# Performance work log

Hardware: AMD Instinct MI355X
Metric: run time of the kernel (lower is better)

The kernel has to match this reference:

```python
import jax, jax.numpy as jnp
import numpy as np
from jax import lax

BN_EPS = 1e-5


def _conv(x, w, pad=0):
    # NCHW / OIHW conv, stride 1
    return lax.conv_general_dilated(
        x, w, (1, 1), [(pad, pad), (pad, pad)],
        dimension_numbers=("NCHW", "OIHW", "NCHW"))


def _bn(x, p):
    # p: [4, C] rows = gamma, beta, running_mean, running_var (eval-mode BN)
    g, b, m, v = p
    inv = g * lax.rsqrt(v + BN_EPS)
    return x * inv[None, :, None, None] + (b - m * inv)[None, :, None, None]


def _avgpool3(x):
    # AvgPool2d(k=3, stride=1, pad=1, count_include_pad=True) -> sum window / 9
    s = lax.reduce_window(x, 0.0, lax.add, (1, 1, 3, 3), (1, 1, 1, 1),
                          [(0, 0), (0, 0), (1, 1), (1, 1)])
    return s / 9.0


def setup_inputs() -> dict:
    key = jax.random.key(0)
    B, C, H, W = 8, 64, 256, 256
    mid = C // 2
    ks = jax.random.split(key, 12)

    def bn_params(k, ch):
        k1, k2, k3, k4 = jax.random.split(k, 4)
        gamma = 1.0 + 0.1 * jax.random.normal(k1, (ch,), jnp.float32)
        beta = 0.1 * jax.random.normal(k2, (ch,), jnp.float32)
        mean = 0.1 * jax.random.normal(k3, (ch,), jnp.float32)
        var = jax.random.uniform(k4, (ch,), jnp.float32, 0.5, 1.5)
        return jnp.stack([gamma, beta, mean, var])

    def w(k, shape):
        fan_in = shape[1] * shape[2] * shape[3]
        return jax.random.normal(k, shape, jnp.float32) / np.sqrt(fan_in)

    return {
        "x": jax.random.normal(ks[0], (B, C, H, W), jnp.float32),
        "w_main": w(ks[1], (mid, C, 3, 3)),
        "bn_main": bn_params(ks[2], mid),
        "w_1x1": w(ks[3], (mid, C, 1, 1)),
        "bn_1x1": bn_params(ks[4], mid),
        "w_3x3_1": w(ks[5], (mid, C, 1, 1)),
        "bn_3x3_1": bn_params(ks[6], mid),
        "w_3x3_2": w(ks[7], (mid, mid, 3, 3)),
        "bn_3x3_2": bn_params(ks[8], mid),
        "w_avg": w(ks[9], (mid, C, 1, 1)),
        "bn_avg_1": bn_params(ks[10], mid),
        "bn_avg_2": bn_params(ks[10], mid),
        "c_score": jax.random.normal(ks[11], (2 * C,), jnp.float32),
    }


def reference(x, w_main, bn_main, w_1x1, bn_1x1, w_3x3_1, bn_3x3_1,
              w_3x3_2, bn_3x3_2, w_avg, bn_avg_1, bn_avg_2, c_score):
    c = x.shape[1]
    # four branches, each -> mid = c//2 channels
    branch_main = _bn(_conv(x, w_main, pad=1), bn_main)
    branch_1x1 = _bn(_conv(x, w_1x1), bn_1x1)
    branch_3x3 = _bn(_conv(_bn(_conv(x, w_3x3_1), bn_3x3_1), w_3x3_2, pad=1), bn_3x3_2)
    branch_avg = _bn(_avgpool3(_bn(_conv(x, w_avg), bn_avg_1)), bn_avg_2)
    out = jnp.concatenate([branch_main, branch_1x1, branch_3x3, branch_avg], axis=1)  # [B, 2c, H, W]

    # top-k channel selection: output channel i = sigmoid(c_score[ind[i]]) * out[:, ind[i]]
    # (the original builds a sparse [c, 2c, 1, 1] conv weight; gather+scale is the same math)
    _, ind = lax.top_k(c_score, c)
    scale = jax.nn.sigmoid(c_score)[ind]                       # [c]
    return jnp.take(out, ind, axis=1) * scale[None, :, None, None]
```

## Files before the change

### kernel.cpp

```cpp
#include <hip/hip_runtime.h>
#include <hip/hip_bf16.h>


typedef __attribute__((ext_vector_type(8))) short bf16x8;
typedef __attribute__((ext_vector_type(16))) float f32x16;
typedef __attribute__((ext_vector_type(4))) unsigned int u32x4;

#define MFMA32(a,b,c) __builtin_amdgcn_mfma_f32_32x32x16_bf16(a,b,c,0,0,0)

#define XT_OFF   131072ull
#define T1_OFF   69877760ull
#define WS_NEED  104751104ull
#define ROWP     264
#define BROW     258

__device__ __forceinline__ unsigned short f2bf(float f) {
    union { __hip_bfloat16 h; unsigned short u; } cv;
    cv.h = __float2bfloat16(f);
    return cv.u;
}

__device__ __forceinline__ f32x16 zero16() {
    f32x16 z;
    #pragma unroll
    for (int i = 0; i < 16; i++) z[i] = 0.f;
    return z;
}

__device__ __forceinline__ int xs_addr(int pos, int byteoff) {
    return pos * 128 + (byteoff ^ (((pos >> 2) & 7) << 4));
}
__device__ __forceinline__ int t1_addr(int pos, int byteoff) {
    return pos * 64 + (byteoff ^ ((pos & 3) << 4));
}

__global__ void prep_kernel(
    const float* __restrict__ c_score,
    const float* __restrict__ w_main, const float* __restrict__ bn_main,
    const float* __restrict__ w_1x1,  const float* __restrict__ bn_1x1,
    const float* __restrict__ w_3x3_1,const float* __restrict__ bn_3x3_1,
    const float* __restrict__ w_3x3_2,const float* __restrict__ bn_3x3_2,
    const float* __restrict__ w_avg,  const float* __restrict__ bn_avg_1,
    const float* __restrict__ bn_avg_2,
    int* __restrict__ och, float* __restrict__ biasb,
    __hip_bfloat16* __restrict__ wb, unsigned char* __restrict__ ws)
{
    const int t = threadIdx.x;
    const int bid = blockIdx.x;

    if (bid >= 4) {
        int gid = (bid - 4) * 256 + t;
        unsigned short* xt = (unsigned short*)(ws + XT_OFF);
        unsigned short* t1 = (unsigned short*)(ws + T1_OFF);
        int which, c, pxid;
        if (gid < 66560) { which = 0; c = gid & 7; pxid = gid >> 3; }
        else if (gid < 99840) { int j = gid - 66560; which = 1; c = j & 3; pxid = j >> 2; }
        else return;
        int b = pxid / 1040, r = pxid - b * 1040;
        int ry, cx;
        if (r < 264)      { ry = 0;             cx = r; }
        else if (r < 528) { ry = 257;           cx = r - 264; }
        else if (r < 784) { ry = 1 + (r - 528); cx = 0; }
        else              { ry = 1 + (r - 784); cx = 257; }
        u32x4 z = {0, 0, 0, 0};
        if (which == 0) {
            size_t ch = ((size_t)(b * BROW + ry) * 8 + c) * ROWP + cx;
            *(u32x4*)(xt + ch * 8) = z;
        } else {
            size_t px = (size_t)(b * BROW + ry) * ROWP + cx;
            *(u32x4*)(t1 + px * 32 + c * 8) = z;
        }
        return;
    }

    __shared__ float ssc[128];
    __shared__ float iv[6][32];

    if (t < 128) ssc[t] = 1.f / (1.f + expf(-c_score[t]));
    if (t < 32) {
        iv[0][t] = bn_main[t]  * rsqrtf(bn_main[96+t]  + 1e-5f);
        iv[1][t] = bn_1x1[t]   * rsqrtf(bn_1x1[96+t]   + 1e-5f);
        iv[2][t] = bn_3x3_1[t] * rsqrtf(bn_3x3_1[96+t] + 1e-5f);
        iv[3][t] = bn_3x3_2[t] * rsqrtf(bn_3x3_2[96+t] + 1e-5f);
        iv[4][t] = bn_avg_1[t] * rsqrtf(bn_avg_1[96+t] + 1e-5f);
        iv[5][t] = bn_avg_2[t] * rsqrtf(bn_avg_2[96+t] + 1e-5f);
    }
    __syncthreads();

    if (bid == 0) {
        if (t < 128) {
            float sj = c_score[t];
            int r = 0;
            for (int i = 0; i < 128; i++) {
                float si = c_score[i];
                r += (si > sj) || (si == sj && i < t);
            }
            och[t] = (r < 64) ? r : -1;
        }
        if (t < 32) {
            biasb[t]     = bn_3x3_1[32+t] - bn_3x3_1[64+t]*iv[2][t];
            biasb[32+t]  = (bn_main[32+t]  - bn_main[64+t]*iv[0][t])  * ssc[t];
            biasb[64+t]  = (bn_1x1[32+t]   - bn_1x1[64+t]*iv[1][t])   * ssc[32+t];
            biasb[96+t]  = (bn_3x3_2[32+t] - bn_3x3_2[64+t]*iv[3][t]) * ssc[64+t];
            biasb[128+t] = (bn_avg_2[32+t] - bn_avg_2[64+t]*iv[5][t]) * ssc[96+t];
            float b1p = bn_avg_1[32+t] - bn_avg_1[64+t]*iv[4][t];
            biasb[160+t] = ssc[96+t] * iv[5][t] * b1p * (1.f/9.f);
        }
    } else if (bid == 1) {
        for (int i = t; i < 2048; i += 256) {
            int j = i & 7, o = (i >> 3) & 31, g = (i >> 8) & 1, s = i >> 9;
            int c = s * 16 + g * 8 + j;
            wb[i]         = __float2bfloat16(w_3x3_1[o*64+c] * iv[2][o]);
            wb[20480 + i] = __float2bfloat16(w_avg[o*64+c] * iv[4][o] * iv[5][o] * (1.f/9.f) * ssc[96+o]);
            wb[22528 + i] = __float2bfloat16(w_1x1[o*64+c] * iv[1][o] * ssc[32+o]);
        }
    } else if (bid == 2) {
        for (int i = t; i < 18432; i += 256) {
            int j = i & 7, o = (i >> 3) & 31, g = (i >> 8) & 1;
            int s = (i >> 9) & 3, tap = i >> 11;
            int c = s * 16 + g * 8 + j;
            wb[2048 + i] = __float2bfloat16(w_main[o*576 + c*9 + tap] * iv[0][o] * ssc[o]);
        }
    } else {
        for (int i = t; i < 9216; i += 256) {
            int j = i & 7, o = (i >> 3) & 31, g = (i >> 8) & 1;
            int s = (i >> 9) & 1, tap = i >> 10;
            int c = s * 16 + g * 8 + j;
            wb[24576 + i] = __float2bfloat16(w_3x3_2[o*288 + c*9 + tap] * iv[3][o] * ssc[64+o]);
        }
    }
}

__global__ __launch_bounds__(256, 8) void t_kernel(
    const float* __restrict__ x, unsigned short* __restrict__ xt)
{
    const int t = threadIdx.x;
    const int co = t >> 5, pq = t & 31;
    const int y = blockIdx.y, b = blockIdx.z;
    const int pxa = blockIdx.x * 128 + pq * 4;

    const float* xp = x + ((size_t)(b * 64 + co * 8) * 65536) + y * 256 + pxa;
    float4 f[8];
    #pragma unroll
    for (int k = 0; k < 8; k++)
        f[k] = *(const float4*)(xp + (size_t)k * 65536);

    size_t xrow = ((size_t)(b * BROW + y + 1) * 8 + co) * ROWP;
    #pragma unroll
    for (int u = 0; u < 4; u++) {
        u32x4 w;
        #pragma unroll
        for (int j = 0; j < 4; j++) {
            const float* a  = (const float*)&f[2*j];
            const float* c2 = (const float*)&f[2*j+1];
            w[j] = (unsigned)f2bf(a[u]) | ((unsigned)f2bf(c2[u]) << 16);
        }
        *(u32x4*)(xt + (xrow + pxa + u + 1) * 8) = w;
    }
}

__global__ __launch_bounds__(256, 8) void m1_kernel(
    const unsigned short* __restrict__ xt,
    const __hip_bfloat16* __restrict__ Wg,
    const float* __restrict__ biasb,
    unsigned short* __restrict__ t1g)
{
    const int t = threadIdx.x;
    const int lane = t & 63, wv = t >> 6;
    const int i31 = lane & 31, g = lane >> 5;
    const int y = blockIdx.y, b = blockIdx.z;
    const int px0 = blockIdx.x * 128, m0 = wv * 32;

    size_t rowb = (size_t)(b * BROW + y + 1) * 8;
    f32x16 acc = zero16();
    #pragma unroll
    for (int s = 0; s < 4; s++) {
        int ch = s * 2 + g;
        bf16x8 a  = *(const bf16x8*)(xt + ((rowb + ch) * ROWP + px0 + m0 + i31 + 1) * 8);
        bf16x8 bA = *(const bf16x8*)(Wg + (ch * 32 + i31) * 8);
        acc = MFMA32(a, bA, acc);
    }
    float bias = biasb[i31];
    size_t trow = (size_t)(b * BROW + y + 1) * ROWP;
    #pragma unroll
    for (int r = 0; r < 16; r++) {
        int px = m0 + (r & 3) + 8 * (r >> 2) + 4 * g;
        t1g[(trow + px0 + px + 1) * 32 + i31] = f2bf(acc[r] + bias);
    }
}

__device__ __forceinline__ void store4(float* outb, const f32x16& acc,
    const int* __restrict__ och_g, const float* __restrict__ bias32,
    int cbase, int y, int x0, int i31, int g)
{
    int rank = och_g[cbase + i31];
    if (rank < 0) return;
    float bias = bias32[i31];
    float* po = outb + (size_t)rank * 65536 + y*256 + x0 + 4*g;
    #pragma unroll
    for (int q = 0; q < 4; q++) {
        float4 v;
        v.x = acc[4*q+0] + bias;
        v.y = acc[4*q+1] + bias;
        v.z = acc[4*q+2] + bias;
        v.w = acc[4*q+3] + bias;
        *(float4*)(po + 8*q) = v;
    }
}

__device__ __forceinline__ void store4avg(float* outb, const f32x16& acc,
    const int* __restrict__ och_g, const float* __restrict__ biasb,
    int y, int x0, int i31, int g)
{
    int rank = och_g[96 + i31];
    if (rank < 0) return;
    float t2b = biasb[128 + i31];
    float b19 = biasb[160 + i31];
    float cy = 3.f - (float)(y == 0) - (float)(y == 255);
    float* po = outb + (size_t)rank * 65536 + y*256 + x0 + 4*g;
    #pragma unroll
    for (int q = 0; q < 4; q++) {
        float4 v;
        #pragma unroll
        for (int u = 0; u < 4; u++) {
            int gx = x0 + 4*g + 8*q + u;
            float cx = 3.f - (float)(gx == 0) - (float)(gx == 255);
            ((float*)&v)[u] = acc[4*q+u] + t2b + b19 * (cy * cx);
        }
        *(float4*)(po + 8*q) = v;
    }
}

__global__ __launch_bounds__(256, 2) void m2ab_kernel(
    const unsigned short* __restrict__ xt,
    const unsigned short* __restrict__ t1g,
    const __hip_bfloat16* __restrict__ Wg,
    const int* __restrict__ och_g,
    const float* __restrict__ biasb,
    float* __restrict__ out)
{
    __shared__ __align__(16) unsigned char smem[43520];

    const int t = threadIdx.x;
    const int lane = t & 63, wv = t >> 6;
    const int i31 = lane & 31, g = lane >> 5;
    const int x0 = blockIdx.x * 32, y0 = blockIdx.y * 8;
    const int zz = blockIdx.z;

    const int y_0 = y0 + 2 * wv, y_1 = y_0 + 1;
    const int r0 = 2 * wv + 1, r1 = r0 + 1;

    if (zz < 8) {
        const int b = zz;
        unsigned short* xs = (unsigned short*)smem;
        {
            u32x4 tmp[11];
            int   jj[11];
            #pragma unroll
            for (int i = 0; i < 11; i++) {
                int j = t + i * 256;
                if (j > 2719) j = 2719;
                jj[i] = j;
                int c = j / 340, rem = j - c * 340, r = rem / 34, p = rem - r * 34;
                size_t src = ((size_t)(b * BROW + y0 + r) * 8 + c) * ROWP + x0 + p;
                tmp[i] = *(const u32x4*)(xt + src * 8);
            }
            #pragma unroll
            for (int i = 0; i < 11; i++)
                *(u32x4*)(xs + (size_t)jj[i] * 8) = tmp[i];
        }
        __syncthreads();

        float* outb = out + (size_t)b * (64 * 65536);
        f32x16 aM0 = zero16(), aM1 = zero16();
        f32x16 aG0 = zero16(), aG1 = zero16();
        f32x16 aX0 = zero16(), aX1 = zero16();
        {
            bf16x8 bg[4], bx[4];
            #pragma unroll
            for (int s = 0; s < 4; s++) {
                bg[s] = *(const bf16x8*)(Wg + 20480 + ((s*2+g)*32 + i31) * 8);
                bx[s] = *(const bf16x8*)(Wg + 22528 + ((s*2+g)*32 + i31) * 8);
            }
            #pragma unroll
            for (int tap = 0; tap < 9; tap++) {
                int dy = tap / 3 - 1, dx = tap - (tap / 3) * 3 - 1;
                int pbase = i31 + dx + 1;
                #pragma unroll
                for (int s = 0; s < 4; s++) {
                    bf16x8 bm = *(const bf16x8*)(Wg + 2048 + (((tap*4+s)*2+g)*32 + i31) * 8);
                    bf16x8 a0 = *(const bf16x8*)(xs + (size_t)(((s*2+g) * 10 + r0 + dy) * 34 + pbase) * 8);
                    bf16x8 a1 = *(const bf16x8*)(xs + (size_t)(((s*2+g) * 10 + r1 + dy) * 34 + pbase) * 8);
                    aM0 = MFMA32(a0, bm, aM0);
                    aM1 = MFMA32(a1, bm, aM1);
                    aG0 = MFMA32(a0, bg[s], aG0);
                    aG1 = MFMA32(a1, bg[s], aG1);
                    if (tap == 4) {
                        aX0 = MFMA32(a0, bx[s], aX0);
                        aX1 = MFMA32(a1, bx[s], aX1);
                    }
                }
            }
        }
        store4(outb, aM0, och_g, biasb + 32, 0,  y_0, x0, i31, g);
        store4(outb, aM1, och_g, biasb + 32, 0,  y_1, x0, i31, g);
        store4(outb, aX0, och_g, biasb + 64, 32, y_0, x0, i31, g);
        store4(outb, aX1, och_g, biasb + 64, 32, y_1, x0, i31, g);
        store4avg(outb, aG0, och_g, biasb, y_0, x0, i31, g);
        store4avg(outb, aG1, och_g, biasb, y_1, x0, i31, g);
    } else {
        const int b = zz - 8;
        unsigned short* t1s = (unsigned short*)smem;
        #pragma unroll
        for (int i = 0; i < 6; i++) {
            int j = t + i * 256;
            if (j > 1359) j = 1359;
            int c4 = j & 3, pr = j >> 2;
            int r = pr / 34, p = pr - r * 34;
            size_t src = ((size_t)(b * BROW + y0 + r) * ROWP + x0 + p) * 32 + c4 * 8;
            int ci = c4 * 350 + r * 35 + p;
            *(u32x4*)(t1s + (size_t)ci * 8) = *(const u32x4*)(t1g + src);
        }
        __syncthreads();

        float* outb = out + (size_t)b * (64 * 65536);
        f32x16 aC0 = zero16(), aC1 = zero16();
        #pragma unroll
        for (int tap = 0; tap < 9; tap++) {
            int dy = tap / 3 - 1, dx = tap - (tap / 3) * 3 - 1;
            int pbase = i31 + dx + 1;
            #pragma unroll
            for (int s = 0; s < 2; s++) {
                bf16x8 bc = *(const bf16x8*)(Wg + 24576 + (((tap*2+s)*2+g)*32 + i31) * 8);
                bf16x8 a0 = *(const bf16x8*)(t1s + (size_t)((s*2+g) * 350 + (r0 + dy) * 35 + pbase) * 8);
                bf16x8 a1 = *(const bf16x8*)(t1s + (size_t)((s*2+g) * 350 + (r1 + dy) * 35 + pbase) * 8);
                aC0 = MFMA32(a0, bc, aC0);
                aC1 = MFMA32(a1, bc, aC1);
            }
        }
        store4(outb, aC0, och_g, biasb + 96, 64, y_0, x0, i31, g);
        store4(outb, aC1, och_g, biasb + 96, 64, y_1, x0, i31, g);
    }
}

__global__ __launch_bounds__(512, 4) void fused_fallback(
    const float* __restrict__ x,
    const __hip_bfloat16* __restrict__ Wg,
    const int* __restrict__ och_g,
    const float* __restrict__ biasb,
    float* __restrict__ out)
{
    __shared__ __align__(16) unsigned char xs[400 * 128];
    __shared__ __align__(16) unsigned char t1s[340 * 64];

    const int t = threadIdx.x;
    const int lane = t & 63, wv = t >> 6;
    const int i31 = lane & 31, g = lane >> 5;
    const int x0 = blockIdx.x * 32, y0 = blockIdx.y * 8;
    const int b = blockIdx.z;

    const float* xb = x + (size_t)b * (64 * 65536);
    for (int j = t; j < 800; j += 512) {
        int co = j / 100;
        int rem = j - co * 100;
        int row = rem / 10, xq = rem - row * 10;
        int gy = y0 - 1 + row;
        int gx0 = x0 - 4 + 4 * xq;
        bool ok = ((unsigned)gy < 256u) && ((unsigned)gx0 <= 252u);
        const float* p = xb + (size_t)(co * 8) * 65536 + (size_t)gy * 256 + gx0;
        float4 f0 = {0,0,0,0}, f1 = {0,0,0,0}, f2 = {0,0,0,0}, f3 = {0,0,0,0};
        float4 f4 = {0,0,0,0}, f5 = {0,0,0,0}, f6 = {0,0,0,0}, f7 = {0,0,0,0};
        if (ok) {
            f0 = *(const float4*)(p);
            f1 = *(const float4*)(p + 65536);
            f2 = *(const float4*)(p + 131072);
            f3 = *(const float4*)(p + 196608);
            f4 = *(const float4*)(p + 262144);
            f5 = *(const float4*)(p + 327680);
            f6 = *(const float4*)(p + 393216);
            f7 = *(const float4*)(p + 458752);
        }
        const float* fv[8] = {(const float*)&f0, (const float*)&f1, (const float*)&f2,
                              (const float*)&f3, (const float*)&f4, (const float*)&f5,
                              (const float*)&f6, (const float*)&f7};
        #pragma unroll
        for (int u = 0; u < 4; u++) {
            int pos = row * 40 + 4 * xq + u;
            u32x4 w;
            w[0] = (unsigned)f2bf(fv[0][u]) | ((unsigned)f2bf(fv[1][u]) << 16);
            w[1] = (unsigned)f2bf(fv[2][u]) | ((unsigned)f2bf(fv[3][u]) << 16);
            w[2] = (unsigned)f2bf(fv[4][u]) | ((unsigned)f2bf(fv[5][u]) << 16);
            w[3] = (unsigned)f2bf(fv[6][u]) | ((unsigned)f2bf(fv[7][u]) << 16);
            *(u32x4*)(xs + xs_addr(pos, co * 16)) = w;
        }
    }
    __syncthreads();

    {
        bf16x8 bA[4];
        #pragma unroll
        for (int s = 0; s < 4; s++)
            bA[s] = *(const bf16x8*)(Wg + ((s*2+g)*32 + i31) * 8);
        float biasA = biasb[i31];
        for (int mt = wv; mt < 11; mt += 8) {
            int m0 = mt * 32;
            f32x16 acc = zero16();
            int qr = m0 + i31; if (qr > 339) qr = 339;
            int hy = qr / 34, hx = qr - hy * 34;
            int pos = hy * 40 + hx + 3;
            #pragma unroll
            for (int s = 0; s < 4; s++) {
                bf16x8 a = *(const bf16x8*)(xs + xs_addr(pos, s * 32 + g * 16));
                acc = MFMA32(a, bA[s], acc);
            }
            #pragma unroll
            for (int r = 0; r < 16; r++) {
                int q = m0 + (r & 3) + 8 * (r >> 2) + 4 * g;
                if (q < 340) {
                    int hy2 = q / 34, hx2 = q - hy2 * 34;
                    int gy = y0 - 1 + hy2, gx = x0 - 1 + hx2;
                    bool valid = ((unsigned)gy < 256u) && ((unsigned)gx < 256u);
                    float vv = valid ? (acc[r] + biasA) : 0.f;
                    *(unsigned short*)(t1s + t1_addr(q, i31 * 2)) = f2bf(vv);
                }
            }
        }
    }
    __syncthreads();

    float* outb = out + (size_t)b * (64 * 65536);
    const int y = y0 + wv;

    f32x16 aM = zero16(), aG = zero16(), aX = zero16();
    {
        bf16x8 bg[4], bx[4];
        #pragma unroll
        for (int s = 0; s < 4; s++) {
            bg[s] = *(const bf16x8*)(Wg + 20480 + ((s*2+g)*32 + i31) * 8);
            bx[s] = *(const bf16x8*)(Wg + 22528 + ((s*2+g)*32 + i31) * 8);
        }
        for (int tap = 0; tap < 9; tap++) {
            int dy = tap / 3 - 1, dx = tap - (tap / 3) * 3 - 1;
            int pos = (wv + 1 + dy) * 40 + 4 + dx + i31;
            #pragma unroll
            for (int s = 0; s < 4; s++) {
                bf16x8 bm = *(const bf16x8*)(Wg + 2048 + (((tap*4+s)*2+g)*32 + i31) * 8);
                bf16x8 a = *(const bf16x8*)(xs + xs_addr(pos, s * 32 + g * 16));
                aM = MFMA32(a, bm, aM);
                aG = MFMA32(a, bg[s], aG);
                if (tap == 4) aX = MFMA32(a, bx[s], aX);
            }
        }
    }
    store4(outb, aM, och_g, biasb + 32, 0,  y, x0, i31, g);
    store4(outb, aX, och_g, biasb + 64, 32, y, x0, i31, g);
    store4avg(outb, aG, och_g, biasb, y, x0, i31, g);

    f32x16 aC = zero16();
    for (int tap = 0; tap < 9; tap++) {
        int dy = tap / 3 - 1, dx = tap - (tap / 3) * 3 - 1;
        int q = (wv + 1 + dy) * 34 + 1 + dx + i31;
        #pragma unroll
        for (int s = 0; s < 2; s++) {
            bf16x8 bc = *(const bf16x8*)(Wg + 24576 + (((tap*2+s)*2+g)*32 + i31) * 8);
            bf16x8 a = *(const bf16x8*)(t1s + t1_addr(q, s * 32 + g * 16));
            aC = MFMA32(a, bc, aC);
        }
    }
    store4(outb, aC, och_g, biasb + 96, 64, y, x0, i31, g);
}

extern "C" void kernel_launch(void* const* d_in, const int* in_sizes, int n_in,
                              void* d_out, int out_size, void* d_ws, size_t ws_size,
                              hipStream_t stream)
{
    const float* x        = (const float*)d_in[0];
    const float* w_main   = (const float*)d_in[1];
    const float* bn_main  = (const float*)d_in[2];
    const float* w_1x1    = (const float*)d_in[3];
    const float* bn_1x1   = (const float*)d_in[4];
    const float* w_3x3_1  = (const float*)d_in[5];
    const float* bn_3x3_1 = (const float*)d_in[6];
    const float* w_3x3_2  = (const float*)d_in[7];
    const float* bn_3x3_2 = (const float*)d_in[8];
    const float* w_avg    = (const float*)d_in[9];
    const float* bn_avg_1 = (const float*)d_in[10];
    const float* bn_avg_2 = (const float*)d_in[11];
    const float* c_score  = (const float*)d_in[12];

    int*   och   = (int*)d_ws;
    float* biasb = (float*)((char*)d_ws + 512);
    __hip_bfloat16* wb = (__hip_bfloat16*)((char*)d_ws + 2048);

    const bool big = (ws_size >= WS_NEED);
    prep_kernel<<<big ? 394 : 4, 256, 0, stream>>>(
        c_score, w_main, bn_main, w_1x1, bn_1x1,
        w_3x3_1, bn_3x3_1, w_3x3_2, bn_3x3_2, w_avg, bn_avg_1, bn_avg_2,
        och, biasb, wb, (unsigned char*)d_ws);

    if (big) {
        unsigned short* xt  = (unsigned short*)((char*)d_ws + XT_OFF);
        unsigned short* t1g = (unsigned short*)((char*)d_ws + T1_OFF);

        t_kernel<<<dim3(2, 256, 8), 256, 0, stream>>>(x, xt);
        m1_kernel<<<dim3(2, 256, 8), 256, 0, stream>>>(xt, wb, biasb, t1g);
        m2ab_kernel<<<dim3(8, 32, 16), 256, 0, stream>>>(
            xt, t1g, wb, och, biasb, (float*)d_out);
    } else {
        fused_fallback<<<dim3(8, 32, 8), 512, 0, stream>>>(
            x, wb, och, biasb, (float*)d_out);
    }
}
```

Before: 143.6 us.

## Move halo zeroing into producer kernels, interleave m2ab branches, raise occupancy

Halo-border zeroing of the transposed input and t1 buffers moves out of the prep kernel and into t_kernel and m1_kernel, so prep launches only 4 blocks. m2ab now interleaves the two branch types by batch (even z for main/1x1/avg, odd z for the 3x3 branch), which mixes heavy and light blocks during scheduling. Its launch bounds rise from 2 to 3 blocks per CU, which may force register spills in the heavy branch.

After: 142.7 us. About the same (-0.6%).

```diff
diff --git a/kernel.cpp b/kernel.cpp
--- a/kernel.cpp
+++ b/kernel.cpp
@@ -43,35 +43,10 @@
     const float* __restrict__ w_avg,  const float* __restrict__ bn_avg_1,
     const float* __restrict__ bn_avg_2,
     int* __restrict__ och, float* __restrict__ biasb,
-    __hip_bfloat16* __restrict__ wb, unsigned char* __restrict__ ws)
+    __hip_bfloat16* __restrict__ wb)
 {
     const int t = threadIdx.x;
     const int bid = blockIdx.x;
-
-    if (bid >= 4) {
-        int gid = (bid - 4) * 256 + t;
-        unsigned short* xt = (unsigned short*)(ws + XT_OFF);
-        unsigned short* t1 = (unsigned short*)(ws + T1_OFF);
-        int which, c, pxid;
-        if (gid < 66560) { which = 0; c = gid & 7; pxid = gid >> 3; }
-        else if (gid < 99840) { int j = gid - 66560; which = 1; c = j & 3; pxid = j >> 2; }
-        else return;
-        int b = pxid / 1040, r = pxid - b * 1040;
-        int ry, cx;
-        if (r < 264)      { ry = 0;             cx = r; }
-        else if (r < 528) { ry = 257;           cx = r - 264; }
-        else if (r < 784) { ry = 1 + (r - 528); cx = 0; }
-        else              { ry = 1 + (r - 784); cx = 257; }
-        u32x4 z = {0, 0, 0, 0};
-        if (which == 0) {
-            size_t ch = ((size_t)(b * BROW + ry) * 8 + c) * ROWP + cx;
-            *(u32x4*)(xt + ch * 8) = z;
-        } else {
-            size_t px = (size_t)(b * BROW + ry) * ROWP + cx;
-            *(u32x4*)(t1 + px * 32 + c * 8) = z;
-        }
-        return;
-    }
 
     __shared__ float ssc[128];
     __shared__ float iv[6][32];
@@ -157,6 +132,23 @@
         }
         *(u32x4*)(xt + (xrow + pxa + u + 1) * 8) = w;
     }
+
+    if (blockIdx.x == 0) {
+        u32x4 z = {0, 0, 0, 0};
+        if (t < 16) {
+            int c = t & 7, side = t >> 3;
+            size_t ch = ((size_t)(b * BROW + y + 1) * 8 + c) * ROWP + (side ? 257 : 0);
+            *(u32x4*)(xt + ch * 8) = z;
+        }
+        if (y < 2) {
+            int ry = (y == 0) ? 0 : 257;
+            for (int j = t; j < 2112; j += 256) {
+                int c = j / 264, cx = j - c * 264;
+                size_t ch = ((size_t)(b * BROW + ry) * 8 + c) * ROWP + cx;
+                *(u32x4*)(xt + ch * 8) = z;
+            }
+        }
+    }
 }
 
 __global__ __launch_bounds__(256, 8) void m1_kernel(
@@ -186,6 +178,23 @@
     for (int r = 0; r < 16; r++) {
         int px = m0 + (r & 3) + 8 * (r >> 2) + 4 * g;
         t1g[(trow + px0 + px + 1) * 32 + i31] = f2bf(acc[r] + bias);
+    }
+
+    if (blockIdx.x == 0) {
+        u32x4 z = {0, 0, 0, 0};
+        if (t < 8) {
+            int c4 = t & 3, side = t >> 2;
+            size_t px = (size_t)(b * BROW + y + 1) * ROWP + (side ? 257 : 0);
+            *(u32x4*)(t1g + px * 32 + c4 * 8) = z;
+        }
+        if (y < 2) {
+            int ry = (y == 0) ? 0 : 257;
+            for (int j = t; j < 1056; j += 256) {
+                int pxi = j >> 2, c4 = j & 3;
+                size_t px = (size_t)(b * BROW + ry) * ROWP + pxi;
+                *(u32x4*)(t1g + px * 32 + c4 * 8) = z;
+            }
+        }
     }
 }
 
@@ -231,7 +240,7 @@
     }
 }
 
-__global__ __launch_bounds__(256, 2) void m2ab_kernel(
+__global__ __launch_bounds__(256, 3) void m2ab_kernel(
     const unsigned short* __restrict__ xt,
     const unsigned short* __restrict__ t1g,
     const __hip_bfloat16* __restrict__ Wg,
@@ -246,12 +255,12 @@
     const int i31 = lane & 31, g = lane >> 5;
     const int x0 = blockIdx.x * 32, y0 = blockIdx.y * 8;
     const int zz = blockIdx.z;
+    const int b = zz >> 1;
 
     const int y_0 = y0 + 2 * wv, y_1 = y_0 + 1;
     const int r0 = 2 * wv + 1, r1 = r0 + 1;
 
-    if (zz < 8) {
-        const int b = zz;
+    if ((zz & 1) == 0) {
         unsigned short* xs = (unsigned short*)smem;
         {
             u32x4 tmp[11];
@@ -309,7 +318,6 @@
         store4avg(outb, aG0, och_g, biasb, y_0, x0, i31, g);
         store4avg(outb, aG1, och_g, biasb, y_1, x0, i31, g);
     } else {
-        const int b = zz - 8;
         unsigned short* t1s = (unsigned short*)smem;
         #pragma unroll
         for (int i = 0; i < 6; i++) {
@@ -492,13 +500,12 @@
     float* biasb = (float*)((char*)d_ws + 512);
     __hip_bfloat16* wb = (__hip_bfloat16*)((char*)d_ws + 2048);
 
-    const bool big = (ws_size >= WS_NEED);
-    prep_kernel<<<big ? 394 : 4, 256, 0, stream>>>(
+    prep_kernel<<<4, 256, 0, stream>>>(
         c_score, w_main, bn_main, w_1x1, bn_1x1,
         w_3x3_1, bn_3x3_1, w_3x3_2, bn_3x3_2, w_avg, bn_avg_1, bn_avg_2,
-        och, biasb, wb, (unsigned char*)d_ws);
-
-    if (big) {
+        och, biasb, wb);
+
+    if (ws_size >= WS_NEED) {
         unsigned short* xt  = (unsigned short*)((char*)d_ws + XT_OFF);
         unsigned short* t1g = (unsigned short*)((char*)d_ws + T1_OFF);
 
```
